# Kernel optimization log

Measured on AMD Instinct MI355X. Metric: run time of the kernel, lower is better.

## Reference

```python
import jax, jax.numpy as jnp
import numpy as np

WIN = 256  # window_size from init_kwargs


def _stream_attn(q, k, v, win, hollow):
    """Banded sliding-window attention.

    hollow=False (s-stream): key j attended iff 0 <= i - j < win (last `win` tokens incl. self).
    hollow=True  (c-stream): key j attended iff win <= i - j < 2*win (tokens [i-2W+1, i-W]).
    Returns (out [B,S,H,D], lse [B,H,S]) with lse = -inf for fully-masked rows.
    """
    B, S, H, D = q.shape
    nb = S // win
    scale = D ** -0.5
    qb = q.reshape(B, nb, win, H, D)
    kb = k.reshape(B, nb, win, H, D)
    vb = v.reshape(B, nb, win, H, D)
    pad = ((0, 0), (2, 0), (0, 0), (0, 0), (0, 0))
    kp = jnp.pad(kb, pad)
    vp = jnp.pad(vb, pad)
    k_ctx = jnp.concatenate([kp[:, t:t + nb] for t in range(3)], axis=2)  # [B,nb,3W,H,D]
    v_ctx = jnp.concatenate([vp[:, t:t + nb] for t in range(3)], axis=2)
    lq = jnp.arange(win)[:, None]
    kk = jnp.arange(3 * win)[None, :]
    t_blk = kk // win
    lk = kk % win
    rel = (2 - t_blk) * win + lq - lk  # i - j, shape [W, 3W]
    if hollow:
        wmask = (rel >= win) & (rel < 2 * win)
    else:
        wmask = (rel >= 0) & (rel < win)
    blk_ok = (jnp.arange(nb)[:, None] - 2 + (jnp.arange(3 * win) // win)[None, :]) >= 0  # [nb,3W]
    mask = wmask[None] & blk_ok[:, None, :]  # [nb, W, 3W]
    logits = jnp.einsum('bnqhd,bnkhd->bnhqk', qb, k_ctx) * scale  # [B,nb,H,W,3W]
    logits = jnp.where(mask[None, :, None], logits, -jnp.inf)
    m = jnp.max(logits, axis=-1)  # [B,nb,H,W]
    ms = jnp.where(jnp.isneginf(m), 0.0, m)
    p = jnp.exp(logits - ms[..., None])
    denom = jnp.sum(p, axis=-1)  # [B,nb,H,W]
    out = jnp.einsum('bnhqk,bnkhd->bnqhd', p, v_ctx)  # [B,nb,W,H,D]
    safe = jnp.where(denom > 0, denom, 1.0)
    out = out / jnp.moveaxis(safe, 2, 3)[..., None]
    lse = jnp.where(denom > 0, jnp.log(safe) + m, -jnp.inf)  # [B,nb,H,W]
    out = out.reshape(B, S, H, D)
    lse = jnp.moveaxis(lse, 1, 2).reshape(B, H, S)
    return out, lse


def _merge(out_c, lse_c, out_s, lse_s):
    # faithful jax version of merge_attn_states_torch (LSE online-softmax merge)
    m = jnp.maximum(lse_c, lse_s)
    ms = jnp.where(jnp.isneginf(m), 0.0, m)
    ec = jnp.exp(lse_c - ms)
    es = jnp.exp(lse_s - ms)
    se = ec + es  # s-stream always has >=1 key (self), so se > 0
    c_scale = jnp.moveaxis(ec / se, 1, 2)[..., None]  # [B,S,H,1]
    s_scale = jnp.moveaxis(es / se, 1, 2)[..., None]
    return out_c * c_scale + out_s * s_scale


def setup_inputs() -> dict:
    key = jax.random.key(0)
    k1, k2, k3 = jax.random.split(key, 3)
    B, S, H, D = 2, 2048, 16, 128
    return {
        'query': jax.random.normal(k1, (B, S, H, D), dtype=jnp.float32),
        'key': jax.random.normal(k2, (B, S, H, D), dtype=jnp.float32),
        'value': jax.random.normal(k3, (B, S, H, D), dtype=jnp.float32),
    }


def reference(query, key, value):
    out_c, lse_c = _stream_attn(query, key, value, WIN, hollow=True)   # c-stream: [i-2W, i-W]
    out_s, lse_s = _stream_attn(query, key, value, WIN, hollow=False)  # s-stream: last W tokens
    return _merge(out_c, lse_c, out_s, lse_s)
```

## Files before the change

### kernel.cpp

```cpp
#include <hip/hip_runtime.h>
#include <math.h>

#define S_LEN 2048
#define NH    16
#define DD    128
#define SROW  (NH*DD)
#define WIN2  512
#define BQ    128
#define BK    32
#define RSQ   136
#define RSV   56
#define RSP   40

typedef __bf16 bf16x8 __attribute__((ext_vector_type(8)));
typedef __bf16 bf16x4 __attribute__((ext_vector_type(4)));
typedef float  f32x4  __attribute__((ext_vector_type(4)));

__device__ __forceinline__ f32x4 mfma16(bf16x8 a, bf16x8 b, f32x4 c) {
    return __builtin_amdgcn_mfma_f32_16x16x32_bf16(a, b, c, 0, 0, 0);
}

__device__ __forceinline__ unsigned int pack_bf16(float lo, float hi) {
    return (unsigned int)__builtin_bit_cast(unsigned short, (__bf16)lo)
         | ((unsigned int)__builtin_bit_cast(unsigned short, (__bf16)hi) << 16);
}

#define OFF_V0 4352
#define OFF_K1 11520
#define OFF_V1 15872
#define OFF_P  23040
#define SMEM_ELEMS 28160

#define LOAD_CHUNK(c) do {                                                    \
    kv0 = *(const float4*)(Kp + (size_t)((c) + kRow     ) * SROW);            \
    kv1 = *(const float4*)(Kp + (size_t)((c) + kRow + 16) * SROW);            \
    vv0 = *(const float4*)(Vp + (size_t)((c) + 0) * SROW);                    \
    vv1 = *(const float4*)(Vp + (size_t)((c) + 2) * SROW); } while (0)

#define CVT_K(v, it, bK) do {                                                 \
    bf16x4 o4_ = { (__bf16)(v).x, (__bf16)(v).y, (__bf16)(v).z, (__bf16)(v).w }; \
    *(bf16x4*)&smem[(bK) + (kRow + (it)*16) * RSQ + kCol] = o4_; } while (0)

#define CVT_V(v4, it, bV) do {                                                \
    const int k0l_ = w*4 + (it)*2;                                            \
    float ox_ = __shfl_xor((v4).x, 32);                                       \
    float oy_ = __shfl_xor((v4).y, 32);                                       \
    float oz_ = __shfl_xor((v4).z, 32);                                       \
    float ow_ = __shfl_xor((v4).w, 32);                                       \
    float lo0_, hi0_, lo1_, hi1_; int d0_;                                    \
    if (gv == 0) { lo0_ = (v4).x; hi0_ = ox_;    lo1_ = (v4).y; hi1_ = oy_;    d0_ = 4*rv; } \
    else         { lo0_ = oz_;    hi0_ = (v4).z; lo1_ = ow_;    hi1_ = (v4).w; d0_ = 4*rv + 2; } \
    int col_ = k0l_ ^ ((rv & 3) << 3);                                        \
    *(unsigned int*)&smem[(bV) + (d0_    ) * RSV + col_] = pack_bf16(lo0_, hi0_); \
    *(unsigned int*)&smem[(bV) + (d0_ + 1) * RSV + col_] = pack_bf16(lo1_, hi1_); } while (0)

#define STAGE_WRITE(bK, bV) do {                                              \
    CVT_K(kv0, 0, bK); CVT_K(kv1, 1, bK);                                     \
    CVT_V(vv0, 0, bV); CVT_V(vv1, 1, bV); } while (0)

__global__ __launch_bounds__(512, 4)
void swattn_kernel(const float* __restrict__ Qg, const float* __restrict__ Kg,
                   const float* __restrict__ Vg, float* __restrict__ Og) {
    __shared__ __align__(16) __bf16 smem[SMEM_ELEMS];

    const int t   = threadIdx.x;
    const int w   = t >> 6;
    const int l   = t & 63;
    const int r16 = l & 15;
    const int g4  = l >> 4;
    const int Qlo = blockIdx.x * BQ;
    const int h   = blockIdx.y;
    const int b   = blockIdx.z;

    const size_t bh = ((size_t)b * S_LEN) * SROW + (size_t)h * DD;
    const float C1 = 0.08838834764831845f * 1.44269504088896340f;

    for (int it = 0; it < 8; ++it) {
        int f   = it * 512 + t;
        int q_l = f >> 5;
        int dq  = (f & 31) * 4;
        const float4 v = *(const float4*)&Qg[bh + (size_t)(Qlo + q_l) * SROW + dq];
        bf16x4 o4 = { (__bf16)(v.x * C1), (__bf16)(v.y * C1),
                      (__bf16)(v.z * C1), (__bf16)(v.w * C1) };
        *(bf16x4*)&smem[q_l * RSQ + dq] = o4;
    }
    __syncthreads();

    bf16x8 qf[4];
#pragma unroll
    for (int sl = 0; sl < 4; ++sl)
        qf[sl] = *(const bf16x8*)&smem[(w*16 + r16) * RSQ + sl*32 + g4*8];
    __syncthreads();

    const f32x4 zero4 = {0.f, 0.f, 0.f, 0.f};
    f32x4 oacc[8];
#pragma unroll
    for (int dg = 0; dg < 8; ++dg) oacc[dg] = zero4;
    float m_run = -1e4f;
    float l_run = 0.f;

    const int q_w = Qlo + w * 16;
    const int gv = l >> 5;
    const int rv = l & 31;

    const int kRow = t >> 5;
    const int kCol = (t & 31) * 4;
    const float* Kp = Kg + bh + kCol;
    const float* Vp = Vg + bh + (size_t)(w*4 + gv) * SROW + 4*rv;

    int cb = Qlo - (WIN2 - 1);
    if (cb < 0) cb = 0;
    cb &= ~(BK - 1);
    const int Qhi = Qlo + BQ - 1;

    float4 kv0, kv1, vv0, vv1;

    LOAD_CHUNK(cb);
    STAGE_WRITE(0, OFF_V0);
    __syncthreads();

    int ph = 0;
    for (int c0 = cb; c0 <= Qhi; c0 += BK) {
        const bool pfn = (c0 + BK <= Qhi);
        if (pfn) LOAD_CHUNK(c0 + BK);

        const int bK = ph ? OFF_K1 : 0;
        const int bV = ph ? OFF_V1 : OFF_V0;

        const bool act = (q_w + 15 >= c0) && (q_w <= c0 + (BK - 1) + (WIN2 - 1));
        if (act) {
            f32x4 st[2] = { zero4, zero4 };
            __builtin_amdgcn_s_setprio(1);
#pragma unroll
            for (int sl = 0; sl < 4; ++sl)
#pragma unroll
                for (int kg = 0; kg < 2; ++kg) {
                    bf16x8 kf = *(const bf16x8*)&smem[bK + (kg*16 + r16) * RSQ + sl*32 + g4*8];
                    st[kg] = mfma16(kf, qf[sl], st[kg]);
                }
            __builtin_amdgcn_s_setprio(0);

            const bool fv = (q_w >= c0 + (BK - 1)) && (q_w + 15 <= c0 + (WIN2 - 1));
            if (!fv) {
                int iq = q_w + r16;
#pragma unroll
                for (int kg = 0; kg < 2; ++kg) {
                    int relb = iq - (c0 + kg*16 + 4*g4);
#pragma unroll
                    for (int rg = 0; rg < 4; ++rg) {
                        bool ok = ((unsigned)(relb - rg)) < (unsigned)WIN2;
                        st[kg][rg] = ok ? st[kg][rg] : -1e30f;
                    }
                }
            }

            float mc = -1e30f;
#pragma unroll
            for (int kg = 0; kg < 2; ++kg)
#pragma unroll
                for (int rg = 0; rg < 4; ++rg) mc = fmaxf(mc, st[kg][rg]);
            mc = fmaxf(mc, __shfl_xor(mc, 16));
            mc = fmaxf(mc, __shfl_xor(mc, 32));
            if (__any(mc - m_run > 8.f)) {
                float mn = fmaxf(m_run, mc);
                float alpha = exp2f(m_run - mn);
                m_run = mn;
                l_run *= alpha;
#pragma unroll
                for (int dg = 0; dg < 8; ++dg)
#pragma unroll
                    for (int rg = 0; rg < 4; ++rg) oacc[dg][rg] *= alpha;
            }
            float sum = 0.f;
#pragma unroll
            for (int kg = 0; kg < 2; ++kg)
#pragma unroll
                for (int rg = 0; rg < 4; ++rg) {
                    float p = exp2f(st[kg][rg] - m_run);
                    st[kg][rg] = p;
                    sum += p;
                }
            sum += __shfl_xor(sum, 16);
            sum += __shfl_xor(sum, 32);
            l_run += sum;

#pragma unroll
            for (int kg = 0; kg < 2; ++kg) {
                f32x4 pv = st[kg];
                bf16x4 p4 = { (__bf16)pv[0], (__bf16)pv[1], (__bf16)pv[2], (__bf16)pv[3] };
                *(bf16x4*)&smem[OFF_P + (w*16 + r16) * RSP + kg*16 + 4*g4] = p4;
            }

            bf16x8 pf = *(const bf16x8*)&smem[OFF_P + (w*16 + r16) * RSP + g4*8];
            __builtin_amdgcn_s_setprio(1);
#pragma unroll
            for (int dg = 0; dg < 8; ++dg) {
                int col = ((g4 ^ (r16 >> 2)) & 3) * 8;
                bf16x8 vf = *(const bf16x8*)&smem[bV + (dg*16 + r16) * RSV + col];
                oacc[dg] = mfma16(vf, pf, oacc[dg]);
            }
            __builtin_amdgcn_s_setprio(0);
        }

        if (pfn) STAGE_WRITE(ph ? 0 : OFF_K1, ph ? OFF_V0 : OFF_V1);
        __syncthreads();
        ph ^= 1;
    }

    float inv = 1.f / l_run;
    int q = q_w + r16;
    size_t base = bh + (size_t)q * SROW;
#pragma unroll
    for (int dg = 0; dg < 8; ++dg) {
        f32x4 o = oacc[dg];
        float4 res = { o[0]*inv, o[1]*inv, o[2]*inv, o[3]*inv };
        *(float4*)&Og[base + dg*16 + 4*g4] = res;
    }
}

extern "C" void kernel_launch(void* const* d_in, const int* in_sizes, int n_in,
                              void* d_out, int out_size, void* d_ws, size_t ws_size,
                              hipStream_t stream) {
    const float* q = (const float*)d_in[0];
    const float* k = (const float*)d_in[1];
    const float* v = (const float*)d_in[2];
    float* o = (float*)d_out;
    int B = in_sizes[0] / (S_LEN * NH * DD);
    dim3 grid(S_LEN / BQ, NH, B);
    swattn_kernel<<<grid, 512, 0, stream>>>(q, k, v, o);
}
```

Before: 168.5 us.

## Give each wave two query sub-tiles to reuse K/V fragments, halve block size

The block shrinks from 8 to 4 waves, and each wave now owns 32 query rows as two 16-row sub-tiles. Each K fragment and V fragment read from LDS therefore feeds two MFMAs, halving LDS read traffic per MFMA. The row-sum shuffle reduction moves out of the inner loop to the epilogue, and the V tile is padded and re-swizzled to avoid bank conflicts. In exchange each thread holds twice as many accumulators and loads, raising register pressure, and there are fewer waves per CU to hide latency.

```diff
diff --git a/kernel.cpp b/kernel.cpp
--- a/kernel.cpp
+++ b/kernel.cpp
@@ -9,7 +9,7 @@
 #define BQ    128
 #define BK    32
 #define RSQ   136
-#define RSV   56
+#define RSV   72
 #define RSP   40
 
 typedef __bf16 bf16x8 __attribute__((ext_vector_type(8)));
@@ -26,23 +26,27 @@
 }
 
 #define OFF_V0 4352
-#define OFF_K1 11520
-#define OFF_V1 15872
-#define OFF_P  23040
-#define SMEM_ELEMS 28160
+#define OFF_K1 13568
+#define OFF_V1 17920
+#define OFF_P  27136
+#define SMEM_ELEMS 32256
 
 #define LOAD_CHUNK(c) do {                                                    \
     kv0 = *(const float4*)(Kp + (size_t)((c) + kRow     ) * SROW);            \
-    kv1 = *(const float4*)(Kp + (size_t)((c) + kRow + 16) * SROW);            \
+    kv1 = *(const float4*)(Kp + (size_t)((c) + kRow +  8) * SROW);            \
+    kv2 = *(const float4*)(Kp + (size_t)((c) + kRow + 16) * SROW);            \
+    kv3 = *(const float4*)(Kp + (size_t)((c) + kRow + 24) * SROW);            \
     vv0 = *(const float4*)(Vp + (size_t)((c) + 0) * SROW);                    \
-    vv1 = *(const float4*)(Vp + (size_t)((c) + 2) * SROW); } while (0)
+    vv1 = *(const float4*)(Vp + (size_t)((c) + 2) * SROW);                    \
+    vv2 = *(const float4*)(Vp + (size_t)((c) + 4) * SROW);                    \
+    vv3 = *(const float4*)(Vp + (size_t)((c) + 6) * SROW); } while (0)
 
 #define CVT_K(v, it, bK) do {                                                 \
     bf16x4 o4_ = { (__bf16)(v).x, (__bf16)(v).y, (__bf16)(v).z, (__bf16)(v).w }; \
-    *(bf16x4*)&smem[(bK) + (kRow + (it)*16) * RSQ + kCol] = o4_; } while (0)
+    *(bf16x4*)&smem[(bK) + (kRow + (it)*8) * RSQ + kCol] = o4_; } while (0)
 
 #define CVT_V(v4, it, bV) do {                                                \
-    const int k0l_ = w*4 + (it)*2;                                            \
+    const int k0l_ = w*8 + (it)*2;                                            \
     float ox_ = __shfl_xor((v4).x, 32);                                       \
     float oy_ = __shfl_xor((v4).y, 32);                                       \
     float oz_ = __shfl_xor((v4).z, 32);                                       \
@@ -50,15 +54,15 @@
     float lo0_, hi0_, lo1_, hi1_; int d0_;                                    \
     if (gv == 0) { lo0_ = (v4).x; hi0_ = ox_;    lo1_ = (v4).y; hi1_ = oy_;    d0_ = 4*rv; } \
     else         { lo0_ = oz_;    hi0_ = (v4).z; lo1_ = ow_;    hi1_ = (v4).w; d0_ = 4*rv + 2; } \
-    int col_ = k0l_ ^ ((rv & 3) << 3);                                        \
+    int col_ = ((((k0l_) >> 3) ^ rv ^ (rv >> 2)) & 3) * 8 + ((k0l_) & 7);     \
     *(unsigned int*)&smem[(bV) + (d0_    ) * RSV + col_] = pack_bf16(lo0_, hi0_); \
     *(unsigned int*)&smem[(bV) + (d0_ + 1) * RSV + col_] = pack_bf16(lo1_, hi1_); } while (0)
 
 #define STAGE_WRITE(bK, bV) do {                                              \
-    CVT_K(kv0, 0, bK); CVT_K(kv1, 1, bK);                                     \
-    CVT_V(vv0, 0, bV); CVT_V(vv1, 1, bV); } while (0)
-
-__global__ __launch_bounds__(512, 4)
+    CVT_K(kv0, 0, bK); CVT_K(kv1, 1, bK); CVT_K(kv2, 2, bK); CVT_K(kv3, 3, bK); \
+    CVT_V(vv0, 0, bV); CVT_V(vv1, 1, bV); CVT_V(vv2, 2, bV); CVT_V(vv3, 3, bV); } while (0)
+
+__global__ __launch_bounds__(256, 2)
 void swattn_kernel(const float* __restrict__ Qg, const float* __restrict__ Kg,
                    const float* __restrict__ Vg, float* __restrict__ Og) {
     __shared__ __align__(16) __bf16 smem[SMEM_ELEMS];
@@ -75,8 +79,8 @@
     const size_t bh = ((size_t)b * S_LEN) * SROW + (size_t)h * DD;
     const float C1 = 0.08838834764831845f * 1.44269504088896340f;
 
-    for (int it = 0; it < 8; ++it) {
-        int f   = it * 512 + t;
+    for (int it = 0; it < 16; ++it) {
+        int f   = it * 256 + t;
         int q_l = f >> 5;
         int dq  = (f & 31) * 4;
         const float4 v = *(const float4*)&Qg[bh + (size_t)(Qlo + q_l) * SROW + dq];
@@ -86,34 +90,38 @@
     }
     __syncthreads();
 
-    bf16x8 qf[4];
-#pragma unroll
-    for (int sl = 0; sl < 4; ++sl)
-        qf[sl] = *(const bf16x8*)&smem[(w*16 + r16) * RSQ + sl*32 + g4*8];
+    bf16x8 qf[2][4];
+#pragma unroll
+    for (int qs = 0; qs < 2; ++qs)
+#pragma unroll
+        for (int sl = 0; sl < 4; ++sl)
+            qf[qs][sl] = *(const bf16x8*)&smem[(w*32 + qs*16 + r16) * RSQ + sl*32 + g4*8];
     __syncthreads();
 
     const f32x4 zero4 = {0.f, 0.f, 0.f, 0.f};
-    f32x4 oacc[8];
-#pragma unroll
-    for (int dg = 0; dg < 8; ++dg) oacc[dg] = zero4;
-    float m_run = -1e4f;
-    float l_run = 0.f;
-
-    const int q_w = Qlo + w * 16;
+    f32x4 oacc[2][8];
+#pragma unroll
+    for (int qs = 0; qs < 2; ++qs)
+#pragma unroll
+        for (int dg = 0; dg < 8; ++dg) oacc[qs][dg] = zero4;
+    float m_run[2] = { -1e4f, -1e4f };
+    float l_part[2] = { 0.f, 0.f };
+
+    const int q_w = Qlo + w * 32;
     const int gv = l >> 5;
     const int rv = l & 31;
 
     const int kRow = t >> 5;
     const int kCol = (t & 31) * 4;
     const float* Kp = Kg + bh + kCol;
-    const float* Vp = Vg + bh + (size_t)(w*4 + gv) * SROW + 4*rv;
+    const float* Vp = Vg + bh + (size_t)(w*8 + gv) * SROW + 4*rv;
 
     int cb = Qlo - (WIN2 - 1);
     if (cb < 0) cb = 0;
     cb &= ~(BK - 1);
     const int Qhi = Qlo + BQ - 1;
 
-    float4 kv0, kv1, vv0, vv1;
+    float4 kv0, kv1, kv2, kv3, vv0, vv1, vv2, vv3;
 
     LOAD_CHUNK(cb);
     STAGE_WRITE(0, OFF_V0);
@@ -127,77 +135,86 @@
         const int bK = ph ? OFF_K1 : 0;
         const int bV = ph ? OFF_V1 : OFF_V0;
 
-        const bool act = (q_w + 15 >= c0) && (q_w <= c0 + (BK - 1) + (WIN2 - 1));
+        const bool act = (q_w + 31 >= c0) && (q_w <= c0 + (BK - 1) + (WIN2 - 1));
         if (act) {
-            f32x4 st[2] = { zero4, zero4 };
+            f32x4 st[2][2];
+#pragma unroll
+            for (int qs = 0; qs < 2; ++qs) { st[qs][0] = zero4; st[qs][1] = zero4; }
             __builtin_amdgcn_s_setprio(1);
 #pragma unroll
-            for (int sl = 0; sl < 4; ++sl)
+            for (int sl = 0; sl < 4; ++sl) {
+                bf16x8 kf0 = *(const bf16x8*)&smem[bK + (r16     ) * RSQ + sl*32 + g4*8];
+                bf16x8 kf1 = *(const bf16x8*)&smem[bK + (16 + r16) * RSQ + sl*32 + g4*8];
+#pragma unroll
+                for (int qs = 0; qs < 2; ++qs) {
+                    st[qs][0] = mfma16(kf0, qf[qs][sl], st[qs][0]);
+                    st[qs][1] = mfma16(kf1, qf[qs][sl], st[qs][1]);
+                }
+            }
+            __builtin_amdgcn_s_setprio(0);
+
+#pragma unroll
+            for (int qs = 0; qs < 2; ++qs) {
+                const int qb = q_w + qs * 16;
+                const bool fv = (qb >= c0 + (BK - 1)) && (qb + 15 <= c0 + (WIN2 - 1));
+                if (!fv) {
+                    int iq = qb + r16;
+#pragma unroll
+                    for (int kg = 0; kg < 2; ++kg) {
+                        int relb = iq - (c0 + kg*16 + 4*g4);
+#pragma unroll
+                        for (int rg = 0; rg < 4; ++rg) {
+                            bool ok = ((unsigned)(relb - rg)) < (unsigned)WIN2;
+                            st[qs][kg][rg] = ok ? st[qs][kg][rg] : -1e30f;
+                        }
+                    }
+                }
+
+                float mc = -1e30f;
+#pragma unroll
+                for (int kg = 0; kg < 2; ++kg)
+#pragma unroll
+                    for (int rg = 0; rg < 4; ++rg) mc = fmaxf(mc, st[qs][kg][rg]);
+                mc = fmaxf(mc, __shfl_xor(mc, 16));
+                mc = fmaxf(mc, __shfl_xor(mc, 32));
+                if (__any(mc - m_run[qs] > 8.f)) {
+                    float mn = fmaxf(m_run[qs], mc);
+                    float alpha = exp2f(m_run[qs] - mn);
+                    m_run[qs] = mn;
+                    l_part[qs] *= alpha;
+#pragma unroll
+                    for (int dg = 0; dg < 8; ++dg)
+#pragma unroll
+                        for (int rg = 0; rg < 4; ++rg) oacc[qs][dg][rg] *= alpha;
+                }
+                float sum = 0.f;
+#pragma unroll
+                for (int kg = 0; kg < 2; ++kg)
+#pragma unroll
+                    for (int rg = 0; rg < 4; ++rg) {
+                        float p = exp2f(st[qs][kg][rg] - m_run[qs]);
+                        st[qs][kg][rg] = p;
+                        sum += p;
+                    }
+                l_part[qs] += sum;
+
 #pragma unroll
                 for (int kg = 0; kg < 2; ++kg) {
-                    bf16x8 kf = *(const bf16x8*)&smem[bK + (kg*16 + r16) * RSQ + sl*32 + g4*8];
-                    st[kg] = mfma16(kf, qf[sl], st[kg]);
-                }
-            __builtin_amdgcn_s_setprio(0);
-
-            const bool fv = (q_w >= c0 + (BK - 1)) && (q_w + 15 <= c0 + (WIN2 - 1));
-            if (!fv) {
-                int iq = q_w + r16;
-#pragma unroll
-                for (int kg = 0; kg < 2; ++kg) {
-                    int relb = iq - (c0 + kg*16 + 4*g4);
-#pragma unroll
-                    for (int rg = 0; rg < 4; ++rg) {
-                        bool ok = ((unsigned)(relb - rg)) < (unsigned)WIN2;
-                        st[kg][rg] = ok ? st[kg][rg] : -1e30f;
-                    }
+                    f32x4 pv = st[qs][kg];
+                    bf16x4 p4 = { (__bf16)pv[0], (__bf16)pv[1], (__bf16)pv[2], (__bf16)pv[3] };
+                    *(bf16x4*)&smem[OFF_P + (w*32 + qs*16 + r16) * RSP + kg*16 + 4*g4] = p4;
                 }
             }
 
-            float mc = -1e30f;
-#pragma unroll
-            for (int kg = 0; kg < 2; ++kg)
-#pragma unroll
-                for (int rg = 0; rg < 4; ++rg) mc = fmaxf(mc, st[kg][rg]);
-            mc = fmaxf(mc, __shfl_xor(mc, 16));
-            mc = fmaxf(mc, __shfl_xor(mc, 32));
-            if (__any(mc - m_run > 8.f)) {
-                float mn = fmaxf(m_run, mc);
-                float alpha = exp2f(m_run - mn);
-                m_run = mn;
-                l_run *= alpha;
-#pragma unroll
-                for (int dg = 0; dg < 8; ++dg)
-#pragma unroll
-                    for (int rg = 0; rg < 4; ++rg) oacc[dg][rg] *= alpha;
-            }
-            float sum = 0.f;
-#pragma unroll
-            for (int kg = 0; kg < 2; ++kg)
-#pragma unroll
-                for (int rg = 0; rg < 4; ++rg) {
-                    float p = exp2f(st[kg][rg] - m_run);
-                    st[kg][rg] = p;
-                    sum += p;
-                }
-            sum += __shfl_xor(sum, 16);
-            sum += __shfl_xor(sum, 32);
-            l_run += sum;
-
-#pragma unroll
-            for (int kg = 0; kg < 2; ++kg) {
-                f32x4 pv = st[kg];
-                bf16x4 p4 = { (__bf16)pv[0], (__bf16)pv[1], (__bf16)pv[2], (__bf16)pv[3] };
-                *(bf16x4*)&smem[OFF_P + (w*16 + r16) * RSP + kg*16 + 4*g4] = p4;
-            }
-
-            bf16x8 pf = *(const bf16x8*)&smem[OFF_P + (w*16 + r16) * RSP + g4*8];
+            bf16x8 pf0 = *(const bf16x8*)&smem[OFF_P + (w*32      + r16) * RSP + g4*8];
+            bf16x8 pf1 = *(const bf16x8*)&smem[OFF_P + (w*32 + 16 + r16) * RSP + g4*8];
             __builtin_amdgcn_s_setprio(1);
 #pragma unroll
             for (int dg = 0; dg < 8; ++dg) {
-                int col = ((g4 ^ (r16 >> 2)) & 3) * 8;
+                int col = ((g4 ^ (r16 >> 2) ^ dg) & 3) * 8;
                 bf16x8 vf = *(const bf16x8*)&smem[bV + (dg*16 + r16) * RSV + col];
-                oacc[dg] = mfma16(vf, pf, oacc[dg]);
+                oacc[0][dg] = mfma16(vf, pf0, oacc[0][dg]);
+                oacc[1][dg] = mfma16(vf, pf1, oacc[1][dg]);
             }
             __builtin_amdgcn_s_setprio(0);
         }
@@ -207,14 +224,20 @@
         ph ^= 1;
     }
 
-    float inv = 1.f / l_run;
-    int q = q_w + r16;
-    size_t base = bh + (size_t)q * SROW;
-#pragma unroll
-    for (int dg = 0; dg < 8; ++dg) {
-        f32x4 o = oacc[dg];
-        float4 res = { o[0]*inv, o[1]*inv, o[2]*inv, o[3]*inv };
-        *(float4*)&Og[base + dg*16 + 4*g4] = res;
+#pragma unroll
+    for (int qs = 0; qs < 2; ++qs) {
+        float lsum = l_part[qs];
+        lsum += __shfl_xor(lsum, 16);
+        lsum += __shfl_xor(lsum, 32);
+        float inv = 1.f / lsum;
+        int q = q_w + qs*16 + r16;
+        size_t base = bh + (size_t)q * SROW;
+#pragma unroll
+        for (int dg = 0; dg < 8; ++dg) {
+            f32x4 o = oacc[qs][dg];
+            float4 res = { o[0]*inv, o[1]*inv, o[2]*inv, o[3]*inv };
+            *(float4*)&Og[base + dg*16 + 4*g4] = res;
+        }
     }
 }
 
@@ -227,5 +250,5 @@
     float* o = (float*)d_out;
     int B = in_sizes[0] / (S_LEN * NH * DD);
     dim3 grid(S_LEN / BQ, NH, B);
-    swattn_kernel<<<grid, 512, 0, stream>>>(q, k, v, o);
-}
+    swattn_kernel<<<grid, 256, 0, stream>>>(q, k, v, o);
+}
```

After: 167.2 us. Within noise of the previous version (-0.8%).

## Halve query tile to 64 rows with 256 threads and XOR-swizzled LDS layouts

Applied to the files above, without the earlier changes.

Shrinks the query block from 128 to 64 rows and the workgroup from 512 to 256 threads, doubling the grid and cutting shared memory per block. Each thread now loads four K and V rows per chunk instead of two. The padded row strides for K/Q and P are replaced with XOR-swizzled layouts, and the V swizzle is changed, to avoid LDS bank conflicts while using less space. The per-row sum reduction is deferred to the end. This raises occupancy and packs the band more tightly, at the cost of each K/V chunk being loaded by more blocks.

```diff
diff --git a/kernel.cpp b/kernel.cpp
--- a/kernel.cpp
+++ b/kernel.cpp
@@ -6,11 +6,9 @@
 #define DD    128
 #define SROW  (NH*DD)
 #define WIN2  512
-#define BQ    128
+#define BQ    64
 #define BK    32
-#define RSQ   136
-#define RSV   56
-#define RSP   40
+#define RSV   40
 
 typedef __bf16 bf16x8 __attribute__((ext_vector_type(8)));
 typedef __bf16 bf16x4 __attribute__((ext_vector_type(4)));
@@ -25,24 +23,31 @@
          | ((unsigned int)__builtin_bit_cast(unsigned short, (__bf16)hi) << 16);
 }
 
-#define OFF_V0 4352
-#define OFF_K1 11520
-#define OFF_V1 15872
-#define OFF_P  23040
-#define SMEM_ELEMS 28160
+#define KQ_OFF(row, col) ((row)*128 + (((((col) >> 3) ^ ((row) & 15)) & 15) << 3) + ((col) & 7))
+#define P_OFF(row, col)  ((row)*32  + (((((col) >> 3) ^ ((row) & 3)) & 3) << 3) + ((col) & 7))
+
+#define OFF_V0 4096
+#define OFF_K1 9216
+#define OFF_V1 13312
+#define OFF_P  18432
+#define SMEM_ELEMS 20480
 
 #define LOAD_CHUNK(c) do {                                                    \
     kv0 = *(const float4*)(Kp + (size_t)((c) + kRow     ) * SROW);            \
-    kv1 = *(const float4*)(Kp + (size_t)((c) + kRow + 16) * SROW);            \
+    kv1 = *(const float4*)(Kp + (size_t)((c) + kRow +  8) * SROW);            \
+    kv2 = *(const float4*)(Kp + (size_t)((c) + kRow + 16) * SROW);            \
+    kv3 = *(const float4*)(Kp + (size_t)((c) + kRow + 24) * SROW);            \
     vv0 = *(const float4*)(Vp + (size_t)((c) + 0) * SROW);                    \
-    vv1 = *(const float4*)(Vp + (size_t)((c) + 2) * SROW); } while (0)
+    vv1 = *(const float4*)(Vp + (size_t)((c) + 2) * SROW);                    \
+    vv2 = *(const float4*)(Vp + (size_t)((c) + 4) * SROW);                    \
+    vv3 = *(const float4*)(Vp + (size_t)((c) + 6) * SROW); } while (0)
 
 #define CVT_K(v, it, bK) do {                                                 \
     bf16x4 o4_ = { (__bf16)(v).x, (__bf16)(v).y, (__bf16)(v).z, (__bf16)(v).w }; \
-    *(bf16x4*)&smem[(bK) + (kRow + (it)*16) * RSQ + kCol] = o4_; } while (0)
+    *(bf16x4*)&smem[(bK) + KQ_OFF(kRow + (it)*8, kCol)] = o4_; } while (0)
 
 #define CVT_V(v4, it, bV) do {                                                \
-    const int k0l_ = w*4 + (it)*2;                                            \
+    const int k0l_ = w*8 + (it)*2;                                            \
     float ox_ = __shfl_xor((v4).x, 32);                                       \
     float oy_ = __shfl_xor((v4).y, 32);                                       \
     float oz_ = __shfl_xor((v4).z, 32);                                       \
@@ -50,15 +55,15 @@
     float lo0_, hi0_, lo1_, hi1_; int d0_;                                    \
     if (gv == 0) { lo0_ = (v4).x; hi0_ = ox_;    lo1_ = (v4).y; hi1_ = oy_;    d0_ = 4*rv; } \
     else         { lo0_ = oz_;    hi0_ = (v4).z; lo1_ = ow_;    hi1_ = (v4).w; d0_ = 4*rv + 2; } \
-    int col_ = k0l_ ^ ((rv & 3) << 3);                                        \
+    int col_ = ((((k0l_) >> 3) ^ rv ^ (rv >> 2)) & 3) * 8 + ((k0l_) & 7);     \
     *(unsigned int*)&smem[(bV) + (d0_    ) * RSV + col_] = pack_bf16(lo0_, hi0_); \
     *(unsigned int*)&smem[(bV) + (d0_ + 1) * RSV + col_] = pack_bf16(lo1_, hi1_); } while (0)
 
 #define STAGE_WRITE(bK, bV) do {                                              \
-    CVT_K(kv0, 0, bK); CVT_K(kv1, 1, bK);                                     \
-    CVT_V(vv0, 0, bV); CVT_V(vv1, 1, bV); } while (0)
-
-__global__ __launch_bounds__(512, 4)
+    CVT_K(kv0, 0, bK); CVT_K(kv1, 1, bK); CVT_K(kv2, 2, bK); CVT_K(kv3, 3, bK); \
+    CVT_V(vv0, 0, bV); CVT_V(vv1, 1, bV); CVT_V(vv2, 2, bV); CVT_V(vv3, 3, bV); } while (0)
+
+__global__ __launch_bounds__(256, 4)
 void swattn_kernel(const float* __restrict__ Qg, const float* __restrict__ Kg,
                    const float* __restrict__ Vg, float* __restrict__ Og) {
     __shared__ __align__(16) __bf16 smem[SMEM_ELEMS];
@@ -76,20 +81,20 @@
     const float C1 = 0.08838834764831845f * 1.44269504088896340f;
 
     for (int it = 0; it < 8; ++it) {
-        int f   = it * 512 + t;
+        int f   = it * 256 + t;
         int q_l = f >> 5;
         int dq  = (f & 31) * 4;
         const float4 v = *(const float4*)&Qg[bh + (size_t)(Qlo + q_l) * SROW + dq];
         bf16x4 o4 = { (__bf16)(v.x * C1), (__bf16)(v.y * C1),
                       (__bf16)(v.z * C1), (__bf16)(v.w * C1) };
-        *(bf16x4*)&smem[q_l * RSQ + dq] = o4;
+        *(bf16x4*)&smem[KQ_OFF(q_l, dq)] = o4;
     }
     __syncthreads();
 
     bf16x8 qf[4];
 #pragma unroll
     for (int sl = 0; sl < 4; ++sl)
-        qf[sl] = *(const bf16x8*)&smem[(w*16 + r16) * RSQ + sl*32 + g4*8];
+        qf[sl] = *(const bf16x8*)&smem[KQ_OFF(w*16 + r16, sl*32 + g4*8)];
     __syncthreads();
 
     const f32x4 zero4 = {0.f, 0.f, 0.f, 0.f};
@@ -97,7 +102,7 @@
 #pragma unroll
     for (int dg = 0; dg < 8; ++dg) oacc[dg] = zero4;
     float m_run = -1e4f;
-    float l_run = 0.f;
+    float l_part = 0.f;
 
     const int q_w = Qlo + w * 16;
     const int gv = l >> 5;
@@ -106,14 +111,14 @@
     const int kRow = t >> 5;
     const int kCol = (t & 31) * 4;
     const float* Kp = Kg + bh + kCol;
-    const float* Vp = Vg + bh + (size_t)(w*4 + gv) * SROW + 4*rv;
+    const float* Vp = Vg + bh + (size_t)(w*8 + gv) * SROW + 4*rv;
 
     int cb = Qlo - (WIN2 - 1);
     if (cb < 0) cb = 0;
     cb &= ~(BK - 1);
     const int Qhi = Qlo + BQ - 1;
 
-    float4 kv0, kv1, vv0, vv1;
+    float4 kv0, kv1, kv2, kv3, vv0, vv1, vv2, vv3;
 
     LOAD_CHUNK(cb);
     STAGE_WRITE(0, OFF_V0);
@@ -135,7 +140,7 @@
             for (int sl = 0; sl < 4; ++sl)
 #pragma unroll
                 for (int kg = 0; kg < 2; ++kg) {
-                    bf16x8 kf = *(const bf16x8*)&smem[bK + (kg*16 + r16) * RSQ + sl*32 + g4*8];
+                    bf16x8 kf = *(const bf16x8*)&smem[bK + KQ_OFF(kg*16 + r16, sl*32 + g4*8)];
                     st[kg] = mfma16(kf, qf[sl], st[kg]);
                 }
             __builtin_amdgcn_s_setprio(0);
@@ -165,7 +170,7 @@
                 float mn = fmaxf(m_run, mc);
                 float alpha = exp2f(m_run - mn);
                 m_run = mn;
-                l_run *= alpha;
+                l_part *= alpha;
 #pragma unroll
                 for (int dg = 0; dg < 8; ++dg)
 #pragma unroll
@@ -180,22 +185,20 @@
                     st[kg][rg] = p;
                     sum += p;
                 }
-            sum += __shfl_xor(sum, 16);
-            sum += __shfl_xor(sum, 32);
-            l_run += sum;
+            l_part += sum;
 
 #pragma unroll
             for (int kg = 0; kg < 2; ++kg) {
                 f32x4 pv = st[kg];
                 bf16x4 p4 = { (__bf16)pv[0], (__bf16)pv[1], (__bf16)pv[2], (__bf16)pv[3] };
-                *(bf16x4*)&smem[OFF_P + (w*16 + r16) * RSP + kg*16 + 4*g4] = p4;
-            }
-
-            bf16x8 pf = *(const bf16x8*)&smem[OFF_P + (w*16 + r16) * RSP + g4*8];
+                *(bf16x4*)&smem[OFF_P + P_OFF(w*16 + r16, kg*16 + 4*g4)] = p4;
+            }
+
+            bf16x8 pf = *(const bf16x8*)&smem[OFF_P + P_OFF(w*16 + r16, g4*8)];
             __builtin_amdgcn_s_setprio(1);
 #pragma unroll
             for (int dg = 0; dg < 8; ++dg) {
-                int col = ((g4 ^ (r16 >> 2)) & 3) * 8;
+                int col = ((g4 ^ (r16 >> 2) ^ dg) & 3) * 8;
                 bf16x8 vf = *(const bf16x8*)&smem[bV + (dg*16 + r16) * RSV + col];
                 oacc[dg] = mfma16(vf, pf, oacc[dg]);
             }
@@ -207,7 +210,10 @@
         ph ^= 1;
     }
 
-    float inv = 1.f / l_run;
+    float lsum = l_part;
+    lsum += __shfl_xor(lsum, 16);
+    lsum += __shfl_xor(lsum, 32);
+    float inv = 1.f / lsum;
     int q = q_w + r16;
     size_t base = bh + (size_t)q * SROW;
 #pragma unroll
@@ -227,5 +233,5 @@
     float* o = (float*)d_out;
     int B = in_sizes[0] / (S_LEN * NH * DD);
     dim3 grid(S_LEN / BQ, NH, B);
-    swattn_kernel<<<grid, 512, 0, stream>>>(q, k, v, o);
-}
+    swattn_kernel<<<grid, 256, 0, stream>>>(q, k, v, o);
+}
```

Measured after the change: 202.0 us. 1.2x slower.
